# Kernel tuning notes

Measured on AMD Instinct MI355X. Metric: run time of the kernel, lower is better.

Reference implementation:

```python
import jax, jax.numpy as jnp
import numpy as np

B, C, H, W = 16, 256, 64, 64
NH, DH = 8, 64
POS_C = 4


def setup_inputs() -> dict:
    key = jax.random.key(0)
    ks = jax.random.split(key, 10)
    cin = C + POS_C
    dqkv = NH * DH
    sc = 1.0 / np.sqrt(cin)
    inp = {
        "x": jax.random.normal(ks[0], (B, C, H, W), dtype=jnp.float32),
        "pos_emb": jax.random.normal(ks[1], (1, POS_C, H, W), dtype=jnp.float32) / np.sqrt(C * H * W),
        "Wk": jax.random.normal(ks[2], (dqkv, cin), dtype=jnp.float32) * sc,
        "bk": jnp.zeros((dqkv,), dtype=jnp.float32),
        "Wq": jax.random.normal(ks[3], (dqkv, cin), dtype=jnp.float32) * sc,
        "bq": jnp.zeros((dqkv,), dtype=jnp.float32),
        "Wv": jax.random.normal(ks[4], (dqkv, cin), dtype=jnp.float32) * sc,
        "bv": jnp.zeros((dqkv,), dtype=jnp.float32),
        "Wo": jax.random.normal(ks[5], (C, dqkv), dtype=jnp.float32) / np.sqrt(dqkv),
        "bo": jnp.zeros((C,), dtype=jnp.float32),
    }
    return inp


def _conv1x1(w, b, x):
    # w: (out, in), x: (B, in, H, W) -> (B, out, H, W)
    return jnp.einsum('oc,bchw->bohw', w, x) + b[None, :, None, None]


def reference(x, pos_emb, Wk, bk, Wq, bq, Wv, bv, Wo, bo):
    b, c, h, w = x.shape
    xp = jnp.concatenate([x, jnp.broadcast_to(pos_emb, (b, POS_C, h, w))], axis=1)
    K = _conv1x1(Wk, bk, xp).reshape(b, NH, DH, h, w)
    Q = _conv1x1(Wq, bq, xp).reshape(b, NH, DH, h, w)
    V = _conv1x1(Wv, bv, xp).reshape(b, NH, DH, h, w)
    # Row (width-axis) logits: (B, nh, H, W, W)
    qk_w = jnp.einsum('bhdij,bhdik->bhijk', Q, K)
    # Column (height-axis) logits: (B, nh, H, W, H)
    qk_h = jnp.einsum('bhdij,bhdkj->bhijk', Q, K)
    scale = 1.0 / np.sqrt(w + h)
    p = jax.nn.softmax(jnp.concatenate([qk_w, qk_h], axis=-1) * scale, axis=-1)
    p_w, p_h = p[..., :w], p[..., w:]
    a_w = jnp.einsum('bhijk,bhdik->bhdij', p_w, V)
    a_h = jnp.einsum('bhijk,bhdkj->bhdij', p_h, V)
    A = (a_w + a_h).reshape(b, NH * DH, h, w)
    return x + _conv1x1(Wo, bo, A)
```

## Files before the change

kernel.cpp:

```cpp
#include <hip/hip_runtime.h>

typedef unsigned short u16;
typedef __bf16 bf16x8 __attribute__((ext_vector_type(8)));
typedef float f32x4 __attribute__((ext_vector_type(4)));
typedef unsigned short u16x8 __attribute__((ext_vector_type(8)));
typedef unsigned short u16x4 __attribute__((ext_vector_type(4)));

#define MFMA16(A,B,C) __builtin_amdgcn_mfma_f32_16x16x32_bf16(A,B,C,0,0,0)

__device__ __forceinline__ float b2f(u16 h){ unsigned u = ((unsigned)h)<<16; return __builtin_bit_cast(float,u); }
__device__ __forceinline__ u16 f2b(float f){ unsigned u = __builtin_bit_cast(unsigned,f); u += 0x7fffu + ((u>>16)&1u); return (u16)(u>>16); }
__device__ __forceinline__ bf16x8 ldb8(const u16* p){ return __builtin_bit_cast(bf16x8, *(const u16x8*)p); }

__device__ __forceinline__ void g2lds16(const u16* g, u16* l){
  __builtin_amdgcn_global_load_lds((const __attribute__((address_space(1))) void*)g,
                                   (__attribute__((address_space(3))) void*)l, 16, 0, 0);
}

#define BAR   __builtin_amdgcn_s_barrier()
#define VMC4  asm volatile("s_waitcnt vmcnt(4)" ::: "memory")
#define VMC0  asm volatile("s_waitcnt vmcnt(0)" ::: "memory")


__global__ void k_prep_w(const float* __restrict__ Wq, const float* __restrict__ Wk,
                         const float* __restrict__ Wv, const float* __restrict__ bq,
                         const float* __restrict__ bk, const float* __restrict__ bv,
                         const float* __restrict__ Wo,
                         u16* __restrict__ WP, u16* __restrict__ BIAS,
                         u16* __restrict__ WoP){
  int r = blockIdx.x;
  int tid = threadIdx.x;
  if (r < 1536){
    int t = r >> 9, rm = r & 511;
    const float* src = (t==0 ? Wq : (t==1 ? Wk : Wv)) + (long)rm*260;
    WP[(long)r*320 + tid] = f2b(src[tid]);
    if (tid < 64) WP[(long)r*320 + 256 + tid] = (tid < 4) ? f2b(src[256 + tid]) : (u16)0;
    if (tid == 0){
      const float* bs = (t==0 ? bq : (t==1 ? bk : bv));
      BIAS[r] = f2b(bs[rm]);
    }
  } else {
    int co = r - 1536;
    WoP[(long)co*512 + tid]       = f2b(Wo[(long)co*512 + tid]);
    WoP[(long)co*512 + 256 + tid] = f2b(Wo[(long)co*512 + 256 + tid]);
  }
}

__global__ void k_sentinel(float* __restrict__ out){
  long i = (long)blockIdx.x*256 + threadIdx.x;
  out[i] = 100.0f;
}

__global__ __launch_bounds__(256) void k_cvtx(const float* __restrict__ x,
                                              const float* __restrict__ pos,
                                              u16* __restrict__ XT, int b0){
  __shared__ u16 tile[64*65];
  int bidx = blockIdx.x;
  int ct = bidx & 3, pt = (bidx>>2)&63, bl = bidx>>8;
  int c0 = ct*64, p0 = pt*64;
  int tid = threadIdx.x;
  const float* xb = x + (long)(b0+bl)*256*4096;
  #pragma unroll
  for (int it=0; it<16; ++it){
    int idx = it*256 + tid; int cc = idx>>6, px = idx&63;
    tile[cc*65 + px] = f2b(xb[(long)(c0+cc)*4096 + p0 + px]);
  }
  __syncthreads();
  u16* dst = XT + ((long)(bl*4096 + p0))*320 + c0;
  #pragma unroll
  for (int it=0; it<4; ++it){
    int idx = it*256 + tid; int pp = idx>>4, c4 = (idx&15)*4;
    u16x4 o;
    #pragma unroll
    for (int u=0;u<4;++u) o[u] = tile[(c4+u)*65 + pp];
    *(u16x4*)&dst[(long)pp*320 + c4] = o;
  }
  if (ct == 0){
    int px = tid>>2, cb = (tid&3)*16;
    u16* row = XT + ((long)(bl*4096 + p0 + px))*320 + 256 + cb;
    #pragma unroll
    for (int half=0; half<2; ++half){
      u16x8 o;
      #pragma unroll
      for (int u=0;u<8;++u){
        int c = cb + half*8 + u;
        o[u] = (c < 4) ? f2b(pos[(long)c*4096 + p0 + px]) : (u16)0;
      }
      *(u16x8*)&row[half*8] = o;
    }
  }
}

__global__ __launch_bounds__(256) void k_qkv(
    const u16* __restrict__ XT, const u16* __restrict__ WP,
    const u16* __restrict__ BIAS,
    u16* __restrict__ Qb, u16* __restrict__ Kb, u16* __restrict__ Vb, int nwg){
  __shared__ u16 sm[32768];
  int hw = blockIdx.x;
  int bidx = (hw & 7)*(nwg >> 3) + (hw >> 3);
  int mt = bidx % 12; long nt = bidx / 12;
  int oc0 = mt*128;
  int bl = (int)(nt >> 5); int pl0 = ((int)nt & 31)*128;
  int tid = threadIdx.x;
  int wid = tid>>6, lane = tid&63, l16 = lane&15, qd = lane>>4;
  int wm = wid>>1, wn = wid&1;
  const u16* gA = WP + (long)oc0*320;
  const u16* gB = XT + ((long)nt*128)*320;

  int b2=(lane>>2)&1, b3=(lane>>3)&1, b4=(lane>>4)&1;
  int lanez = lane ^ ((b2^b4) | (b3<<1) | (b4<<2));
  int srowz = lanez>>2, scolz = (lanez&3)*8;

  f32x4 zf = {0.f,0.f,0.f,0.f};
  f32x4 acc[4][4];
  #pragma unroll
  for (int i=0;i<4;++i){
    #pragma unroll
    for (int j=0;j<4;++j) acc[i][j] = zf;
  }

  auto stage2 = [&](const u16* g, int ldsOff){
    g2lds16(g + (long)(wid*16 + srowz)*320 + scolz,       &sm[ldsOff + wid*512]);
    g2lds16(g + (long)(64 + wid*16 + srowz)*320 + scolz,  &sm[ldsOff + 2048 + wid*512]);
  };
  auto aOff = [&](int buf,int ks){ return (buf*2+ks)*4096; };
  auto bOff = [&](int buf,int ks){ return 16384 + (buf*2+ks)*4096; };
  auto swz = [&](int row, int q){ int byt = (row*64 + q*16) ^ ((row&7)<<4); return byt>>1; };

  bf16x8 rA[4], rB[4];
  auto ldA4 = [&](int buf,int ks){
    int o = aOff(buf,ks);
    #pragma unroll
    for (int i=0;i<4;++i) rA[i] = ldb8(&sm[o + swz(wm*64 + i*16 + l16, qd)]);
  };
  auto ldB4 = [&](int buf,int ks){
    int o = bOff(buf,ks);
    #pragma unroll
    for (int i=0;i<4;++i) rB[i] = ldb8(&sm[o + swz(wn*64 + i*16 + l16, qd)]);
  };
  auto mmac = [&](){
    __builtin_amdgcn_s_setprio(1);
    #pragma unroll
    for (int i=0;i<4;++i){
      #pragma unroll
      for (int j=0;j<4;++j)
        acc[i][j] = MFMA16(rA[i], rB[j], acc[i][j]);
    }
    __builtin_amdgcn_s_setprio(0);
  };

  stage2(gA + 0,  aOff(0,0));
  stage2(gB + 0,  bOff(0,0));
  stage2(gA + 32, aOff(0,1));
  stage2(gB + 32, bOff(0,1));
  VMC4; BAR;

  for (int t=0; t<5; ++t){
    int cur = t&1, nxt = cur^1;
    bool st = (t < 4);
    int k1 = (t+1)*64;
    ldA4(cur,0); ldB4(cur,0);
    if (st){ stage2(gA + k1, aOff(nxt,0)); stage2(gB + k1, bOff(nxt,0)); }
    BAR; mmac();
    if (st) { VMC4; } else { VMC0; }
    BAR;
    ldA4(cur,1); ldB4(cur,1);
    if (st){ stage2(gA + k1 + 32, aOff(nxt,1)); stage2(gB + k1 + 32, bOff(nxt,1)); }
    BAR; mmac();
    if (st) VMC4;
    BAR;
  }

  u16* dstb = (oc0 < 512) ? Qb : (oc0 < 1024 ? Kb : Vb);
  #pragma unroll
  for (int mi=0;mi<4;++mi){
    int oc = oc0 + wm*64 + mi*16 + qd*4;
    int ocm = oc & 511;
    int hh = ocm>>6, dd = ocm&63;
    float bv4[4];
    #pragma unroll
    for (int r=0;r<4;++r) bv4[r] = b2f(BIAS[oc + r]);
    #pragma unroll
    for (int ni=0;ni<4;++ni){
      int pl = pl0 + wn*64 + ni*16 + l16;
      u16x4 pk;
      #pragma unroll
      for (int r=0;r<4;++r) pk[r] = f2b(acc[mi][ni][r] + bv4[r]);
      *(u16x4*)&dstb[((long)(bl*8+hh)*4096 + pl)*64 + dd] = pk;
    }
  }
}

template<int COL>
__global__ __launch_bounds__(256) void k_attn(
    const u16* __restrict__ Qb, const u16* __restrict__ Kb,
    const u16* __restrict__ Vsrc, u16* __restrict__ U,
    float* __restrict__ M, float* __restrict__ L){
  __shared__ u16 sm[4*64*72];
  u16* Qs = sm;
  u16* Ks = sm + 4608;
  u16* VT = sm + 9216;
  u16* Ps = sm + 13824;
  int bid = blockIdx.x;
  int rc = bid&63, h=(bid>>6)&7, bl=bid>>9;
  long plane  = (long)(bl*8+h)*262144;
  long sbase  = (long)(bl*8+h)*4096;
  int tid = threadIdx.x;
  #pragma unroll
  for (int it=0; it<2; ++it){
    int idx = it*256 + tid; int row = idx>>3, c8 = (idx&7)*8;
    long gqk = plane + ((long)(COL ? (row*64 + rc) : (rc*64 + row)))*64 + c8;
    *(u16x8*)&Qs[row*72 + c8] = *(const u16x8*)&Qb[gqk];
    *(u16x8*)&Ks[row*72 + c8] = *(const u16x8*)&Kb[gqk];
    u16x8 v = *(const u16x8*)&Vsrc[gqk];
    int xr = row ^ ((idx&7)<<3);
    #pragma unroll
    for (int u=0;u<8;++u) VT[(c8+u)*72 + xr] = v[u];
  }
  __syncthreads();
  int wid = tid>>6, lane = tid&63, l16 = lane&15, qd = lane>>4;
  int j0 = wid*16;
  f32x4 zf = {0.f,0.f,0.f,0.f};
  f32x4 sv[4] = {zf,zf,zf,zf};
  #pragma unroll
  for (int d0=0; d0<64; d0+=32){
    bf16x8 a = ldb8(&Qs[(j0+l16)*72 + d0 + qd*8]);
    #pragma unroll
    for (int n=0;n<4;++n){
      bf16x8 bb = ldb8(&Ks[(n*16+l16)*72 + d0 + qd*8]);
      sv[n] = MFMA16(a, bb, sv[n]);
    }
  }
  const float scale = 0.08838834764831845f;
  float mrow[4], lrow[4];
  #pragma unroll
  for (int r=0;r<4;++r){
    float mv = -1e30f;
    #pragma unroll
    for (int n=0;n<4;++n){ sv[n][r] *= scale; mv = fmaxf(mv, sv[n][r]); }
    mv = fmaxf(mv, __shfl_xor(mv,1)); mv = fmaxf(mv, __shfl_xor(mv,2));
    mv = fmaxf(mv, __shfl_xor(mv,4)); mv = fmaxf(mv, __shfl_xor(mv,8));
    float ls = 0.f;
    #pragma unroll
    for (int n=0;n<4;++n){ float p = expf(fminf(sv[n][r]-mv, 0.f)); sv[n][r] = p; ls += p; }
    ls += __shfl_xor(ls,1); ls += __shfl_xor(ls,2);
    ls += __shfl_xor(ls,4); ls += __shfl_xor(ls,8);
    mrow[r]=mv; lrow[r]=ls;
    int qi = j0 + qd*4 + r;
    #pragma unroll
    for (int n=0;n<4;++n) Ps[qi*72 + n*16 + l16] = f2b(sv[n][r]);
  }
  __syncthreads();
  f32x4 u4[4] = {zf,zf,zf,zf};
  #pragma unroll
  for (int k0=0;k0<64;k0+=32){
    bf16x8 a = ldb8(&Ps[(j0+l16)*72 + k0 + qd*8]);
    #pragma unroll
    for (int n=0;n<4;++n){
      int dd = n*16 + l16;
      bf16x8 bb = ldb8(&VT[dd*72 + ((k0 + qd*8) ^ (((dd>>3)&7)<<3))]);
      u4[n] = MFMA16(a, bb, u4[n]);
    }
  }
  if (!COL){
    #pragma unroll
    for (int r=0;r<4;++r){
      int qi = j0 + qd*4 + r;
      long pl = (long)rc*64 + qi;
      long ob = (sbase + pl)*64;
      #pragma unroll
      for (int n=0;n<4;++n) U[ob + n*16 + l16] = f2b(u4[n][r]);
      if (l16==0){ M[sbase+pl]=mrow[r]; L[sbase+pl]=lrow[r]; }
    }
  } else {
    #pragma unroll
    for (int r=0;r<4;++r){
      int qi = j0 + qd*4 + r;
      long pix = sbase + (long)qi*64 + rc;
      float mw = M[pix], lw = L[pix];
      float mh = mrow[r], lh = lrow[r];
      float m  = fmaxf(mw, mh);
      float ew = expf(fminf(mw - m, 0.f));
      float eh = expf(fminf(mh - m, 0.f));
      float rden = 1.f / fmaxf(ew*lw + eh*lh, 1e-20f);
      long ob = pix*64;
      #pragma unroll
      for (int n=0;n<4;++n){
        float uw = b2f(U[ob + n*16 + l16]);
        U[ob + n*16 + l16] = f2b((ew*uw + eh*u4[n][r])*rden);
      }
    }
  }
}

__global__ __launch_bounds__(256) void k_oproj(
    const u16* __restrict__ WoP, const float* __restrict__ bo,
    const u16* __restrict__ AC, const float* __restrict__ x,
    float* __restrict__ out, int b0){
  __shared__ u16 sW[128*32];
  __shared__ u16 sA[128*32];
  int bidx = blockIdx.x;
  int mt = bidx & 1; long nt = bidx >> 1;
  int co0 = mt*128; long p0 = nt*128;
  int bl = (int)(p0>>12), pl0 = (int)(p0&4095);
  int gb = b0 + bl;
  int tid = threadIdx.x;
  int wid=tid>>6, lane=tid&63, l16=lane&15, qd=lane>>4;
  int wm=wid>>1, wn=wid&1;
  int srow = lane>>2, sc8 = (lane&3)*8;
  f32x4 zf = {0.f,0.f,0.f,0.f};
  f32x4 acc[4][4];
  #pragma unroll
  for (int i=0;i<4;++i){
    #pragma unroll
    for (int j=0;j<4;++j) acc[i][j] = zf;
  }
  for (int kk=0; kk<512; kk+=32){
    __syncthreads();
    #pragma unroll
    for (int c=0;c<2;++c){
      int seg = wid*2 + c;
      int row = seg*16 + srow;
      g2lds16(&WoP[(long)(co0+row)*512 + kk + sc8], &sW[seg*512]);
      g2lds16(&AC[((long)(bl*8+(kk>>6))*4096 + pl0 + row)*64 + (kk&63) + sc8], &sA[seg*512]);
    }
    __syncthreads();
    bf16x8 a[4], bb[4];
    #pragma unroll
    for (int mi=0;mi<4;++mi) a[mi]  = ldb8(&sW[(wm*64+mi*16+l16)*32 + qd*8]);
    #pragma unroll
    for (int ni=0;ni<4;++ni) bb[ni] = ldb8(&sA[(wn*64+ni*16+l16)*32 + qd*8]);
    #pragma unroll
    for (int mi=0;mi<4;++mi){
      #pragma unroll
      for (int ni=0;ni<4;++ni)
        acc[mi][ni] = MFMA16(a[mi], bb[ni], acc[mi][ni]);
    }
  }
  #pragma unroll
  for (int mi=0;mi<4;++mi){
    #pragma unroll
    for (int ni=0;ni<4;++ni){
      int n = wn*64+ni*16+l16; int pl = pl0+n;
      #pragma unroll
      for (int r=0;r<4;++r){
        int co = co0 + wm*64+mi*16+qd*4+r;
        long addr = ((long)(gb*256+co))*4096 + pl;
        out[addr] = acc[mi][ni][r] + bo[co] + x[addr];
      }
    }
  }
}

extern "C" void kernel_launch(void* const* d_in, const int* in_sizes, int n_in,
                              void* d_out, int out_size, void* d_ws, size_t ws_size,
                              hipStream_t stream) {
  (void)in_sizes; (void)n_in; (void)out_size;
  const float* x    = (const float*)d_in[0];
  const float* pos  = (const float*)d_in[1];
  const float* Wk   = (const float*)d_in[2];
  const float* bk   = (const float*)d_in[3];
  const float* Wq   = (const float*)d_in[4];
  const float* bq   = (const float*)d_in[5];
  const float* Wv   = (const float*)d_in[6];
  const float* bv   = (const float*)d_in[7];
  const float* Wo   = (const float*)d_in[8];
  const float* bo   = (const float*)d_in[9];
  float* out = (float*)d_out;
  char* ws = (char*)d_ws;

  const long per_batch = 19660800l;
  const long fixed = 1248256l;
  if (fixed + per_batch > (long)ws_size){
    k_sentinel<<<65536, 256, 0, stream>>>(out);
    return;
  }
  int CB = 16;
  while (CB > 1 && fixed + (long)CB*per_batch > (long)ws_size) CB >>= 1;

  u16*  WP   = (u16*)(ws);
  u16*  BIAS = (u16*)(ws + 983040l);
  u16*  WoP  = (u16*)(ws + 986112l);
  long base  = fixed;
  u16*  XT   = (u16*)(ws + base);
  u16*  Qc   = (u16*)(ws + base + (long)CB*2621440l);
  u16*  Kc   = (u16*)((char*)Qc  + (long)CB*4194304l);
  u16*  Vc   = (u16*)((char*)Kc  + (long)CB*4194304l);
  u16*  Uw   = (u16*)((char*)Vc  + (long)CB*4194304l);
  float* MWc = (float*)((char*)Uw + (long)CB*4194304l);
  float* LWc = (float*)((char*)MWc + (long)CB*131072l);

  k_prep_w<<<1792, 256, 0, stream>>>(Wq, Wk, Wv, bq, bk, bv, Wo, WP, BIAS, WoP);
  for (int b0 = 0; b0 < 16; b0 += CB){
    k_cvtx    <<<CB*256, 256, 0, stream>>>(x, pos, XT, b0);
    k_qkv     <<<CB*384, 256, 0, stream>>>(XT, WP, BIAS, Qc, Kc, Vc, CB*384);
    k_attn<0> <<<CB*512, 256, 0, stream>>>(Qc, Kc, Vc, Uw, MWc, LWc);
    k_attn<1> <<<CB*512, 256, 0, stream>>>(Qc, Kc, Vc, Uw, MWc, LWc);
    k_oproj   <<<CB*64,  256, 0, stream>>>(WoP, bo, Uw, x, out, b0);
  }
}
```

Measured before the change: 403.3 us.

## Fuse x transpose and bf16 conversion into QKV GEMM B-operand staging

Removes the separate k_cvtx kernel and its XT workspace. The QKV GEMM now loads fp32 x and pos directly into registers, converts them to bf16 and writes them swizzled into LDS, software-pipelined alongside the async weight loads, with new vmcnt waits. This drops one launch and a write-then-read of the transposed activation. In exchange, each x tile is reloaded by all 12 output-channel tiles as fp32, which is twice the bytes of bf16, and the kernel gains register pressure and VALU work.

```diff
diff --git a/kernel.cpp b/kernel.cpp
--- a/kernel.cpp
+++ b/kernel.cpp
@@ -17,9 +17,11 @@
                                    (__attribute__((address_space(3))) void*)l, 16, 0, 0);
 }
 
-#define BAR   __builtin_amdgcn_s_barrier()
-#define VMC4  asm volatile("s_waitcnt vmcnt(4)" ::: "memory")
-#define VMC0  asm volatile("s_waitcnt vmcnt(0)" ::: "memory")
+#define BAR    __builtin_amdgcn_s_barrier()
+#define LGKM0  asm volatile("s_waitcnt lgkmcnt(0)" ::: "memory")
+#define VMC18  asm volatile("s_waitcnt vmcnt(18)" ::: "memory")
+#define VMC2   asm volatile("s_waitcnt vmcnt(2)"  ::: "memory")
+#define VMC0   asm volatile("s_waitcnt vmcnt(0)"  ::: "memory")
 
 
 __global__ void k_prep_w(const float* __restrict__ Wq, const float* __restrict__ Wk,
@@ -51,50 +53,11 @@
   out[i] = 100.0f;
 }
 
-__global__ __launch_bounds__(256) void k_cvtx(const float* __restrict__ x,
-                                              const float* __restrict__ pos,
-                                              u16* __restrict__ XT, int b0){
-  __shared__ u16 tile[64*65];
-  int bidx = blockIdx.x;
-  int ct = bidx & 3, pt = (bidx>>2)&63, bl = bidx>>8;
-  int c0 = ct*64, p0 = pt*64;
-  int tid = threadIdx.x;
-  const float* xb = x + (long)(b0+bl)*256*4096;
-  #pragma unroll
-  for (int it=0; it<16; ++it){
-    int idx = it*256 + tid; int cc = idx>>6, px = idx&63;
-    tile[cc*65 + px] = f2b(xb[(long)(c0+cc)*4096 + p0 + px]);
-  }
-  __syncthreads();
-  u16* dst = XT + ((long)(bl*4096 + p0))*320 + c0;
-  #pragma unroll
-  for (int it=0; it<4; ++it){
-    int idx = it*256 + tid; int pp = idx>>4, c4 = (idx&15)*4;
-    u16x4 o;
-    #pragma unroll
-    for (int u=0;u<4;++u) o[u] = tile[(c4+u)*65 + pp];
-    *(u16x4*)&dst[(long)pp*320 + c4] = o;
-  }
-  if (ct == 0){
-    int px = tid>>2, cb = (tid&3)*16;
-    u16* row = XT + ((long)(bl*4096 + p0 + px))*320 + 256 + cb;
-    #pragma unroll
-    for (int half=0; half<2; ++half){
-      u16x8 o;
-      #pragma unroll
-      for (int u=0;u<8;++u){
-        int c = cb + half*8 + u;
-        o[u] = (c < 4) ? f2b(pos[(long)c*4096 + p0 + px]) : (u16)0;
-      }
-      *(u16x8*)&row[half*8] = o;
-    }
-  }
-}
-
 __global__ __launch_bounds__(256) void k_qkv(
-    const u16* __restrict__ XT, const u16* __restrict__ WP,
-    const u16* __restrict__ BIAS,
-    u16* __restrict__ Qb, u16* __restrict__ Kb, u16* __restrict__ Vb, int nwg){
+    const float* __restrict__ x, const float* __restrict__ pos,
+    const u16* __restrict__ WP, const u16* __restrict__ BIAS,
+    u16* __restrict__ Qb, u16* __restrict__ Kb, u16* __restrict__ Vb,
+    int nwg, int b0){
   __shared__ u16 sm[32768];
   int hw = blockIdx.x;
   int bidx = (hw & 7)*(nwg >> 3) + (hw >> 3);
@@ -104,8 +67,8 @@
   int tid = threadIdx.x;
   int wid = tid>>6, lane = tid&63, l16 = lane&15, qd = lane>>4;
   int wm = wid>>1, wn = wid&1;
-  const u16* gA = WP + (long)oc0*320;
-  const u16* gB = XT + ((long)nt*128)*320;
+  const u16*   gA = WP + (long)oc0*320;
+  const float* xq = x + (long)(b0+bl)*256*4096;
 
   int b2=(lane>>2)&1, b3=(lane>>3)&1, b4=(lane>>4)&1;
   int lanez = lane ^ ((b2^b4) | (b3<<1) | (b4<<2));
@@ -119,13 +82,40 @@
     for (int j=0;j<4;++j) acc[i][j] = zf;
   }
 
-  auto stage2 = [&](const u16* g, int ldsOff){
+  auto stageA = [&](int kk, int ldsOff){
+    const u16* g = gA + kk;
     g2lds16(g + (long)(wid*16 + srowz)*320 + scolz,       &sm[ldsOff + wid*512]);
     g2lds16(g + (long)(64 + wid*16 + srowz)*320 + scolz,  &sm[ldsOff + 2048 + wid*512]);
   };
   auto aOff = [&](int buf,int ks){ return (buf*2+ks)*4096; };
   auto bOff = [&](int buf,int ks){ return 16384 + (buf*2+ks)*4096; };
-  auto swz = [&](int row, int q){ int byt = (row*64 + q*16) ^ ((row&7)<<4); return byt>>1; };
+  auto swz  = [&](int row, int q){ int byt = (row*64 + q*16) ^ ((row&7)<<4); return byt>>1; };
+
+  int px = tid & 127, chalf = (tid>>7)*16;
+  auto issueX = [&](float* R, int c0){
+    #pragma unroll
+    for (int j=0;j<8;++j){
+      int c = c0 + chalf + 2*j;
+      if (c < 256){
+        R[2*j]   = xq[(long)c*4096 + pl0 + px];
+        R[2*j+1] = xq[(long)c*4096 + 4096 + pl0 + px];
+      } else if (c < 260){
+        R[2*j]   = pos[(long)(c-256)*4096 + pl0 + px];
+        R[2*j+1] = pos[(long)(c-255)*4096 + pl0 + px];
+      } else {
+        R[2*j] = 0.f; R[2*j+1] = 0.f;
+      }
+    }
+  };
+  auto writeX = [&](const float* R, int ldsOff){
+    #pragma unroll
+    for (int j=0;j<8;++j){
+      int cl = chalf + 2*j;
+      unsigned pk = (unsigned)f2b(R[2*j]) | ((unsigned)f2b(R[2*j+1])<<16);
+      int byt = (px*64 + cl*2) ^ ((px&7)<<4);
+      *(unsigned*)&sm[ldsOff + (byt>>1)] = pk;
+    }
+  };
 
   bf16x8 rA[4], rB[4];
   auto ldA4 = [&](int buf,int ks){
@@ -149,26 +139,32 @@
     __builtin_amdgcn_s_setprio(0);
   };
 
-  stage2(gA + 0,  aOff(0,0));
-  stage2(gB + 0,  bOff(0,0));
-  stage2(gA + 32, aOff(0,1));
-  stage2(gB + 32, bOff(0,1));
-  VMC4; BAR;
-
+  float Ra[16], Rb[16];
+  stageA(0,  aOff(0,0));
+  stageA(32, aOff(0,1));
+  issueX(Ra, 0);
+  VMC0;
+  writeX(Ra, bOff(0,0));
+  issueX(Rb, 32);
+  LGKM0; BAR;
+
+  #pragma unroll
   for (int t=0; t<5; ++t){
     int cur = t&1, nxt = cur^1;
     bool st = (t < 4);
     int k1 = (t+1)*64;
     ldA4(cur,0); ldB4(cur,0);
-    if (st){ stage2(gA + k1, aOff(nxt,0)); stage2(gB + k1, bOff(nxt,0)); }
-    BAR; mmac();
-    if (st) { VMC4; } else { VMC0; }
-    BAR;
+    if (st){ issueX(Ra, k1); stageA(k1, aOff(nxt,0)); }
+    if (t < 3) { VMC18; } else if (t == 3) { VMC2; } else { VMC0; }
+    writeX(Rb, bOff(cur,1));
+    mmac();
+    LGKM0; BAR;
     ldA4(cur,1); ldB4(cur,1);
-    if (st){ stage2(gA + k1 + 32, aOff(nxt,1)); stage2(gB + k1 + 32, bOff(nxt,1)); }
-    BAR; mmac();
-    if (st) VMC4;
-    BAR;
+    if (st){ issueX(Rb, k1+32); stageA(k1+32, aOff(nxt,1)); }
+    if (t < 3) { VMC18; } else if (t == 3) { VMC2; }
+    if (st) writeX(Ra, bOff(nxt,0));
+    mmac();
+    if (st){ LGKM0; BAR; }
   }
 
   u16* dstb = (oc0 < 512) ? Qb : (oc0 < 1024 ? Kb : Vb);
@@ -369,7 +365,7 @@
   float* out = (float*)d_out;
   char* ws = (char*)d_ws;
 
-  const long per_batch = 19660800l;
+  const long per_batch = 17039360l;
   const long fixed = 1248256l;
   if (fixed + per_batch > (long)ws_size){
     k_sentinel<<<65536, 256, 0, stream>>>(out);
@@ -382,8 +378,7 @@
   u16*  BIAS = (u16*)(ws + 983040l);
   u16*  WoP  = (u16*)(ws + 986112l);
   long base  = fixed;
-  u16*  XT   = (u16*)(ws + base);
-  u16*  Qc   = (u16*)(ws + base + (long)CB*2621440l);
+  u16*  Qc   = (u16*)(ws + base);
   u16*  Kc   = (u16*)((char*)Qc  + (long)CB*4194304l);
   u16*  Vc   = (u16*)((char*)Kc  + (long)CB*4194304l);
   u16*  Uw   = (u16*)((char*)Vc  + (long)CB*4194304l);
@@ -392,8 +387,7 @@
 
   k_prep_w<<<1792, 256, 0, stream>>>(Wq, Wk, Wv, bq, bk, bv, Wo, WP, BIAS, WoP);
   for (int b0 = 0; b0 < 16; b0 += CB){
-    k_cvtx    <<<CB*256, 256, 0, stream>>>(x, pos, XT, b0);
-    k_qkv     <<<CB*384, 256, 0, stream>>>(XT, WP, BIAS, Qc, Kc, Vc, CB*384);
+    k_qkv     <<<CB*384, 256, 0, stream>>>(x, pos, WP, BIAS, Qc, Kc, Vc, CB*384, b0);
     k_attn<0> <<<CB*512, 256, 0, stream>>>(Qc, Kc, Vc, Uw, MWc, LWc);
     k_attn<1> <<<CB*512, 256, 0, stream>>>(Qc, Kc, Vc, Uw, MWc, LWc);
     k_oproj   <<<CB*64,  256, 0, stream>>>(WoP, bo, Uw, x, out, b0);
```

Result: slower. 550.9 us (+36.6%).

## Use a 4-slot LDS ring with 3-deep prefetch in the QKV projection GEMM

Applied to the files above, without the earlier changes.

The QKV projection GEMM's K loop moves from a double buffer, with two barriers per 32-wide half-step, to a four-slot LDS ring. Three k-slices are kept in flight and there is one barrier per k-step. The vmcnt waits are adjusted so each step waits only for its own slice. This is meant to hide more global-to-LDS load latency and cut synchronization overhead. LDS usage stays the same, but correctness now depends on the exact vmcnt counting.

```diff
diff --git a/kernel.cpp b/kernel.cpp
--- a/kernel.cpp
+++ b/kernel.cpp
@@ -18,6 +18,7 @@
 }
 
 #define BAR   __builtin_amdgcn_s_barrier()
+#define VMC8  asm volatile("s_waitcnt vmcnt(8)" ::: "memory")
 #define VMC4  asm volatile("s_waitcnt vmcnt(4)" ::: "memory")
 #define VMC0  asm volatile("s_waitcnt vmcnt(0)" ::: "memory")
 
@@ -119,22 +120,26 @@
     for (int j=0;j<4;++j) acc[i][j] = zf;
   }
 
-  auto stage2 = [&](const u16* g, int ldsOff){
-    g2lds16(g + (long)(wid*16 + srowz)*320 + scolz,       &sm[ldsOff + wid*512]);
-    g2lds16(g + (long)(64 + wid*16 + srowz)*320 + scolz,  &sm[ldsOff + 2048 + wid*512]);
-  };
-  auto aOff = [&](int buf,int ks){ return (buf*2+ks)*4096; };
-  auto bOff = [&](int buf,int ks){ return 16384 + (buf*2+ks)*4096; };
+  auto stageA = [&](int kk, int buf){
+    const u16* g = gA + kk;
+    g2lds16(g + (long)(wid*16 + srowz)*320 + scolz,       &sm[buf*4096 + wid*512]);
+    g2lds16(g + (long)(64 + wid*16 + srowz)*320 + scolz,  &sm[buf*4096 + 2048 + wid*512]);
+  };
+  auto stageB = [&](int kk, int buf){
+    const u16* g = gB + kk;
+    g2lds16(g + (long)(wid*16 + srowz)*320 + scolz,       &sm[16384 + buf*4096 + wid*512]);
+    g2lds16(g + (long)(64 + wid*16 + srowz)*320 + scolz,  &sm[16384 + buf*4096 + 2048 + wid*512]);
+  };
   auto swz = [&](int row, int q){ int byt = (row*64 + q*16) ^ ((row&7)<<4); return byt>>1; };
 
   bf16x8 rA[4], rB[4];
-  auto ldA4 = [&](int buf,int ks){
-    int o = aOff(buf,ks);
+  auto ldA4 = [&](int buf){
+    int o = buf*4096;
     #pragma unroll
     for (int i=0;i<4;++i) rA[i] = ldb8(&sm[o + swz(wm*64 + i*16 + l16, qd)]);
   };
-  auto ldB4 = [&](int buf,int ks){
-    int o = bOff(buf,ks);
+  auto ldB4 = [&](int buf){
+    int o = 16384 + buf*4096;
     #pragma unroll
     for (int i=0;i<4;++i) rB[i] = ldb8(&sm[o + swz(wn*64 + i*16 + l16, qd)]);
   };
@@ -149,26 +154,17 @@
     __builtin_amdgcn_s_setprio(0);
   };
 
-  stage2(gA + 0,  aOff(0,0));
-  stage2(gB + 0,  bOff(0,0));
-  stage2(gA + 32, aOff(0,1));
-  stage2(gB + 32, bOff(0,1));
-  VMC4; BAR;
-
-  for (int t=0; t<5; ++t){
-    int cur = t&1, nxt = cur^1;
-    bool st = (t < 4);
-    int k1 = (t+1)*64;
-    ldA4(cur,0); ldB4(cur,0);
-    if (st){ stage2(gA + k1, aOff(nxt,0)); stage2(gB + k1, bOff(nxt,0)); }
-    BAR; mmac();
-    if (st) { VMC4; } else { VMC0; }
+  stageA(0,  0); stageB(0,  0);
+  stageA(32, 1); stageB(32, 1);
+  stageA(64, 2); stageB(64, 2);
+
+  #pragma unroll
+  for (int p=0; p<10; ++p){
+    if (p < 8) { VMC8; } else if (p == 8) { VMC4; } else { VMC0; }
     BAR;
-    ldA4(cur,1); ldB4(cur,1);
-    if (st){ stage2(gA + k1 + 32, aOff(nxt,1)); stage2(gB + k1 + 32, bOff(nxt,1)); }
-    BAR; mmac();
-    if (st) VMC4;
-    BAR;
+    ldA4(p&3); ldB4(p&3);
+    if (p < 7){ stageA((p+3)*32, (p+3)&3); stageB((p+3)*32, (p+3)&3); }
+    mmac();
   }
 
   u16* dstb = (oc0 < 512) ? Qb : (oc0 < 1024 ? Kb : Vb);
```

New measurement: 409.4 us. Within noise of the previous version (+1.5%).
